# Kernel tuning notes

Hardware: AMD Instinct MI355X
Metric: run time of the kernel (lower is better)

The kernel has to match this reference:

```python
import jax, jax.numpy as jnp
import numpy as np

N, NQ, M, DQ, DK, DV, H = 4, 512, 512, 256, 256, 256, 256


def setup_inputs() -> dict:
    key = jax.random.key(0)
    ks = jax.random.split(key, 6)
    scale_q = 1.0 / np.sqrt(DQ)
    scale_k = 1.0 / np.sqrt(DK)
    scale_v = 1.0 / np.sqrt(H)
    return {
        "query": jax.random.normal(ks[0], (N, NQ, DQ), jnp.float32),
        "key": jax.random.normal(ks[1], (N, M, DK), jnp.float32),
        "value": jax.random.normal(ks[2], (N, M, DV), jnp.float32),
        "W_q": jax.random.normal(ks[3], (DQ, H), jnp.float32) * scale_q,
        "W_k": jax.random.normal(ks[4], (DK, H), jnp.float32) * scale_k,
        "W_v": jax.random.normal(ks[5], (H,), jnp.float32) * scale_v,
    }


def reference(query, key, value, W_q, W_k, W_v):
    # project: (N, n, H) and (N, m, H)
    q = jnp.einsum("bnd,dh->bnh", query, W_q)
    k = jnp.einsum("bmd,dh->bmh", key, W_k)
    # broadcast add -> (N, n, m, H), tanh, project H->1 -> scores (N, n, m)
    scores = jnp.einsum("bnmh,h->bnm", jnp.tanh(q[:, :, None, :] + k[:, None, :, :]), W_v)
    attn = jax.nn.softmax(scores, axis=-1)  # (N, n, m)
    return jnp.einsum("bnm,bmv->bnv", attn, value)
```

## Files before the change

kernel.cpp:

```cpp
#include <hip/hip_runtime.h>
#include <hip/hip_bf16.h>

#define NB 4
#define NQL 512
#define ML 512
#define DDIM 256
#define HDIM 256

static constexpr float TWO_LOG2E = 2.8853900817779268f;
static constexpr float LOG2E     = 1.4426950408889634f;

__global__ __launch_bounds__(256) void proj_kernel(
    const float* __restrict__ q_src, const float* __restrict__ k_src,
    const float* __restrict__ Wq,    const float* __restrict__ Wk,
    float* __restrict__ EqT,         float* __restrict__ EkT)
{
    const int z = blockIdx.z;
    const int b = z & 3;
    const int which = z >> 2;
    const float* __restrict__ src  = which ? k_src : q_src;
    const float* __restrict__ W    = which ? Wk    : Wq;
    float* __restrict__       outT = which ? EkT   : EqT;

    const int l0 = blockIdx.x * 32;
    const int h0 = blockIdx.y * 64;
    const int t  = threadIdx.x;
    const int tx = t & 15;
    const int ty = t >> 4;

    __shared__ float sX[32][36];
    __shared__ float sW[32][68];

    float acc[2][4];
    #pragma unroll
    for (int i = 0; i < 2; i++)
        #pragma unroll
        for (int j = 0; j < 4; j++) acc[i][j] = 0.f;

    const int llA = t >> 3, dgA = t & 7;
    const int ddB = t >> 3, hgB = t & 7;

    for (int d0 = 0; d0 < DDIM; d0 += 32) {
        float4 xv = *(const float4*)&src[(size_t)(b * NQL + l0 + llA) * DDIM + d0 + dgA * 4];
        const float* wrow = &W[(size_t)(d0 + ddB) * HDIM + h0 + hgB * 8];
        float4 wa = ((const float4*)wrow)[0];
        float4 wb = ((const float4*)wrow)[1];
        __syncthreads();
        sX[dgA * 4 + 0][llA] = xv.x;
        sX[dgA * 4 + 1][llA] = xv.y;
        sX[dgA * 4 + 2][llA] = xv.z;
        sX[dgA * 4 + 3][llA] = xv.w;
        *(float4*)&sW[ddB][hgB * 8]     = wa;
        *(float4*)&sW[ddB][hgB * 8 + 4] = wb;
        __syncthreads();
        #pragma unroll
        for (int dd = 0; dd < 32; dd++) {
            float4 w4 = *(const float4*)&sW[dd][tx * 4];
            float2 x2 = *(const float2*)&sX[dd][ty * 2];
            acc[0][0] = fmaf(x2.x, w4.x, acc[0][0]);
            acc[0][1] = fmaf(x2.x, w4.y, acc[0][1]);
            acc[0][2] = fmaf(x2.x, w4.z, acc[0][2]);
            acc[0][3] = fmaf(x2.x, w4.w, acc[0][3]);
            acc[1][0] = fmaf(x2.y, w4.x, acc[1][0]);
            acc[1][1] = fmaf(x2.y, w4.y, acc[1][1]);
            acc[1][2] = fmaf(x2.y, w4.z, acc[1][2]);
            acc[1][3] = fmaf(x2.y, w4.w, acc[1][3]);
        }
    }

    #pragma unroll
    for (int j = 0; j < 4; j++) {
        float2 o;
        o.x = __builtin_amdgcn_exp2f(acc[0][j] * TWO_LOG2E);
        o.y = __builtin_amdgcn_exp2f(acc[1][j] * TWO_LOG2E);
        *(float2*)&outT[(size_t)(b * HDIM + h0 + tx * 4 + j) * NQL + l0 + ty * 2] = o;
    }
}

__global__ __launch_bounds__(256) void scores_kernel(
    const float* __restrict__ EqT, const float* __restrict__ EkT,
    const float* __restrict__ Wv, float* __restrict__ P,
    float* __restrict__ Spart)
{
    const int b  = blockIdx.z;
    const int mt = blockIdx.x;
    const int m0 = mt * 64;
    const int n0 = blockIdx.y * 32;
    const int t  = threadIdx.x;
    const int tx = t & 15;
    const int ty = t >> 4;

    __shared__ float sK[32][68];

    float acc0[4] = {}, acc1[4] = {};
    float swv = 0.f;

    const int hhK = t >> 3, ckK = t & 7;

    const float* qcol = &EqT[(size_t)b * HDIM * NQL + n0 + ty * 2];

    for (int h0 = 0; h0 < HDIM; h0 += 32) {
        const float* krow = &EkT[(size_t)(b * HDIM + h0 + hhK) * ML + m0 + ckK * 8];
        float4 ka = ((const float4*)krow)[0];
        float4 kb = ((const float4*)krow)[1];
        __syncthreads();
        *(float4*)&sK[hhK][ckK * 8]     = ka;
        *(float4*)&sK[hhK][ckK * 8 + 4] = kb;
        __syncthreads();
        #pragma unroll 8
        for (int hh = 0; hh < 32; hh++) {
            float2 q2 = *(const float2*)(qcol + (size_t)(h0 + hh) * NQL);
            float4 k4 = *(const float4*)&sK[hh][tx * 4];
            const float wv = Wv[h0 + hh];
            swv += wv;
            const float nw2 = -2.0f * wv;
            {
                float a0 = fmaf(q2.x, k4.x, 1.0f);
                float a1 = fmaf(q2.x, k4.y, 1.0f);
                float a2 = fmaf(q2.x, k4.z, 1.0f);
                float a3 = fmaf(q2.x, k4.w, 1.0f);
                float r01 = __builtin_amdgcn_rcpf(a0 * a1);
                float r23 = __builtin_amdgcn_rcpf(a2 * a3);
                float t01 = nw2 * r01, t23 = nw2 * r23;
                acc0[0] = fmaf(t01, a1, acc0[0]);
                acc0[1] = fmaf(t01, a0, acc0[1]);
                acc0[2] = fmaf(t23, a3, acc0[2]);
                acc0[3] = fmaf(t23, a2, acc0[3]);
            }
            {
                float a0 = fmaf(q2.y, k4.x, 1.0f);
                float a1 = fmaf(q2.y, k4.y, 1.0f);
                float a2 = fmaf(q2.y, k4.z, 1.0f);
                float a3 = fmaf(q2.y, k4.w, 1.0f);
                float r01 = __builtin_amdgcn_rcpf(a0 * a1);
                float r23 = __builtin_amdgcn_rcpf(a2 * a3);
                float t01 = nw2 * r01, t23 = nw2 * r23;
                acc1[0] = fmaf(t01, a1, acc1[0]);
                acc1[1] = fmaf(t01, a0, acc1[1]);
                acc1[2] = fmaf(t23, a3, acc1[2]);
                acc1[3] = fmaf(t23, a2, acc1[3]);
            }
        }
    }

    float rs0, rs1;
    {
        float4 p;
        p.x = __builtin_amdgcn_exp2f((swv + acc0[0]) * LOG2E);
        p.y = __builtin_amdgcn_exp2f((swv + acc0[1]) * LOG2E);
        p.z = __builtin_amdgcn_exp2f((swv + acc0[2]) * LOG2E);
        p.w = __builtin_amdgcn_exp2f((swv + acc0[3]) * LOG2E);
        *(float4*)&P[(size_t)(b * NQL + n0 + ty * 2 + 0) * ML + m0 + tx * 4] = p;
        rs0 = (p.x + p.y) + (p.z + p.w);
    }
    {
        float4 p;
        p.x = __builtin_amdgcn_exp2f((swv + acc1[0]) * LOG2E);
        p.y = __builtin_amdgcn_exp2f((swv + acc1[1]) * LOG2E);
        p.z = __builtin_amdgcn_exp2f((swv + acc1[2]) * LOG2E);
        p.w = __builtin_amdgcn_exp2f((swv + acc1[3]) * LOG2E);
        *(float4*)&P[(size_t)(b * NQL + n0 + ty * 2 + 1) * ML + m0 + tx * 4] = p;
        rs1 = (p.x + p.y) + (p.z + p.w);
    }
    #pragma unroll
    for (int off = 1; off < 16; off <<= 1) {
        rs0 += __shfl_xor(rs0, off);
        rs1 += __shfl_xor(rs1, off);
    }
    if (tx == 0) {
        Spart[(size_t)(mt * NB + b) * NQL + n0 + ty * 2 + 0] = rs0;
        Spart[(size_t)(mt * NB + b) * NQL + n0 + ty * 2 + 1] = rs1;
    }
}

__global__ __launch_bounds__(256) void av_kernel(
    const float* __restrict__ P, const float* __restrict__ Spart,
    const float* __restrict__ V, float* __restrict__ O)
{
    const int b  = blockIdx.z;
    const int v0 = blockIdx.x * 64;
    const int n0 = blockIdx.y * 16;
    const int t  = threadIdx.x;
    const int tx = t & 15;
    const int ty = t >> 4;

    __shared__ float sV[32][68];
    __shared__ float sInv[16];

    if (t < 16) {
        float s = 0.f;
        #pragma unroll
        for (int mt = 0; mt < 8; ++mt)
            s += Spart[(size_t)(mt * NB + b) * NQL + n0 + t];
        sInv[t] = 1.0f / s;
    }

    float4 acc = {0.f, 0.f, 0.f, 0.f};

    const int mmB = t >> 3, vgB = t & 7;
    const float* prow = &P[(size_t)(b * NQL + n0 + ty) * ML];

    const float* vrow0 = &V[(size_t)(b * ML + mmB) * DDIM + v0 + vgB * 8];
    float4 va = ((const float4*)vrow0)[0];
    float4 vb = ((const float4*)vrow0)[1];

    for (int m0 = 0; m0 < ML; m0 += 32) {
        __syncthreads();
        *(float4*)&sV[mmB][vgB * 8]     = va;
        *(float4*)&sV[mmB][vgB * 8 + 4] = vb;
        __syncthreads();
        if (m0 + 32 < ML) {
            const float* vrow = &V[(size_t)(b * ML + m0 + 32 + mmB) * DDIM + v0 + vgB * 8];
            va = ((const float4*)vrow)[0];
            vb = ((const float4*)vrow)[1];
        }
        #pragma unroll
        for (int mg = 0; mg < 8; ++mg) {
            float4 a4 = *(const float4*)&prow[m0 + mg * 4];
            float4 w0 = *(const float4*)&sV[mg * 4 + 0][tx * 4];
            float4 w1 = *(const float4*)&sV[mg * 4 + 1][tx * 4];
            float4 w2 = *(const float4*)&sV[mg * 4 + 2][tx * 4];
            float4 w3 = *(const float4*)&sV[mg * 4 + 3][tx * 4];
            acc.x = fmaf(a4.x, w0.x, acc.x);
            acc.y = fmaf(a4.x, w0.y, acc.y);
            acc.z = fmaf(a4.x, w0.z, acc.z);
            acc.w = fmaf(a4.x, w0.w, acc.w);
            acc.x = fmaf(a4.y, w1.x, acc.x);
            acc.y = fmaf(a4.y, w1.y, acc.y);
            acc.z = fmaf(a4.y, w1.z, acc.z);
            acc.w = fmaf(a4.y, w1.w, acc.w);
            acc.x = fmaf(a4.z, w2.x, acc.x);
            acc.y = fmaf(a4.z, w2.y, acc.y);
            acc.z = fmaf(a4.z, w2.z, acc.z);
            acc.w = fmaf(a4.z, w2.w, acc.w);
            acc.x = fmaf(a4.w, w3.x, acc.x);
            acc.y = fmaf(a4.w, w3.y, acc.y);
            acc.z = fmaf(a4.w, w3.z, acc.z);
            acc.w = fmaf(a4.w, w3.w, acc.w);
        }
    }

    const float inv = sInv[ty];
    float4 o;
    o.x = acc.x * inv;
    o.y = acc.y * inv;
    o.z = acc.z * inv;
    o.w = acc.w * inv;
    *(float4*)&O[(size_t)(b * NQL + n0 + ty) * DDIM + v0 + tx * 4] = o;
}

extern "C" void kernel_launch(void* const* d_in, const int* in_sizes, int n_in,
                              void* d_out, int out_size, void* d_ws, size_t ws_size,
                              hipStream_t stream)
{
    const float* query = (const float*)d_in[0];
    const float* key   = (const float*)d_in[1];
    const float* value = (const float*)d_in[2];
    const float* Wq    = (const float*)d_in[3];
    const float* Wk    = (const float*)d_in[4];
    const float* Wv    = (const float*)d_in[5];
    float* out = (float*)d_out;

    float* EqT   = (float*)d_ws;
    float* EkT   = EqT + (size_t)NB * HDIM * NQL;
    float* P     = EkT + (size_t)NB * HDIM * ML;
    float* Spart = P + (size_t)NB * NQL * ML;

    dim3 gProj(NQL / 32, HDIM / 64, NB * 2);
    proj_kernel<<<gProj, 256, 0, stream>>>(query, key, Wq, Wk, EqT, EkT);

    dim3 gSc(ML / 64, NQL / 32, NB);
    scores_kernel<<<gSc, 256, 0, stream>>>(EqT, EkT, Wv, P, Spart);

    dim3 gAv(DDIM / 64, NQL / 16, NB);
    av_kernel<<<gAv, 256, 0, stream>>>(P, Spart, value, out);
}
```

Measured before the change: 134.9 us.

## Stage Q tile in LDS and double-buffer Q/K with register prefetch

The scores kernel now loads the Q slice into shared memory alongside K, instead of reading it from global memory inside the inner loop. Both tiles are double-buffered, and the next chunk is prefetched into registers while the current one is computed. This drops one of the two barriers per chunk. It aims to cut global load latency in the inner loop and overlap memory traffic with the tanh/rcp math, at the cost of extra LDS use.

```diff
diff --git a/kernel.cpp b/kernel.cpp
--- a/kernel.cpp
+++ b/kernel.cpp
@@ -90,27 +90,41 @@
     const int tx = t & 15;
     const int ty = t >> 4;
 
-    __shared__ float sK[32][68];
+    __shared__ float sQ[2][32][36];
+    __shared__ float sK[2][32][68];
 
     float acc0[4] = {}, acc1[4] = {};
     float swv = 0.f;
 
+    const int hhA = t >> 3, cgA = t & 7;
     const int hhK = t >> 3, ckK = t & 7;
 
-    const float* qcol = &EqT[(size_t)b * HDIM * NQL + n0 + ty * 2];
-
-    for (int h0 = 0; h0 < HDIM; h0 += 32) {
-        const float* krow = &EkT[(size_t)(b * HDIM + h0 + hhK) * ML + m0 + ckK * 8];
-        float4 ka = ((const float4*)krow)[0];
-        float4 kb = ((const float4*)krow)[1];
-        __syncthreads();
-        *(float4*)&sK[hhK][ckK * 8]     = ka;
-        *(float4*)&sK[hhK][ckK * 8 + 4] = kb;
-        __syncthreads();
+    const float* qbase = &EqT[(size_t)b * HDIM * NQL + n0];
+    const float* kbase = &EkT[(size_t)b * HDIM * ML + m0];
+
+    float4 qv = *(const float4*)(qbase + (size_t)hhA * NQL + cgA * 4);
+    const float* kr0 = kbase + (size_t)hhK * ML + ckK * 8;
+    float4 ka = ((const float4*)kr0)[0];
+    float4 kb = ((const float4*)kr0)[1];
+
+    int cur = 0;
+    for (int c = 0; c < 8; ++c) {
+        *(float4*)&sQ[cur][hhA][cgA * 4]     = qv;
+        *(float4*)&sK[cur][hhK][ckK * 8]     = ka;
+        *(float4*)&sK[cur][hhK][ckK * 8 + 4] = kb;
+        __syncthreads();
+        if (c < 7) {
+            const float* qn = qbase + (size_t)((c + 1) * 32 + hhA) * NQL;
+            qv = *(const float4*)(qn + cgA * 4);
+            const float* kn = kbase + (size_t)((c + 1) * 32 + hhK) * ML + ckK * 8;
+            ka = ((const float4*)kn)[0];
+            kb = ((const float4*)kn)[1];
+        }
+        const int h0 = c * 32;
         #pragma unroll 8
         for (int hh = 0; hh < 32; hh++) {
-            float2 q2 = *(const float2*)(qcol + (size_t)(h0 + hh) * NQL);
-            float4 k4 = *(const float4*)&sK[hh][tx * 4];
+            float2 q2 = *(const float2*)&sQ[cur][hh][ty * 2];
+            float4 k4 = *(const float4*)&sK[cur][hh][tx * 4];
             const float wv = Wv[h0 + hh];
             swv += wv;
             const float nw2 = -2.0f * wv;
@@ -141,6 +155,7 @@
                 acc1[3] = fmaf(t23, a2, acc1[3]);
             }
         }
+        cur ^= 1;
     }
 
     float rs0, rs1;
```

After: 130.8 us. -3.0%, faster.
